# Kernel optimization log

Hardware: AMD Instinct MI355X
Metric: run time of the kernel (lower is better)

## Reference

```python
import jax, jax.numpy as jnp
import numpy as np

B, S, H, I, E = 2, 2048, 1024, 4096, 8
NUM_STEPS = 2
RMS_EPS = 1e-6


def rmsnorm(x, w, eps=RMS_EPS):
    var = jnp.mean(jnp.square(x), axis=-1, keepdims=True)
    return x * jax.lax.rsqrt(var + eps) * w


def setup_inputs() -> dict:
    key = jax.random.key(0)
    ks = jax.random.split(key, 7)
    return {
        "hidden_states": jax.random.normal(ks[0], (B, S, H), dtype=jnp.float32),
        "gate_w": jax.random.normal(ks[1], (E, H), dtype=jnp.float32) * 0.02,
        "w1": jax.random.normal(ks[2], (E, H, I), dtype=jnp.float32) * 0.02,
        "b1": jnp.zeros((E, I), dtype=jnp.float32),
        "w2": jax.random.normal(ks[3], (E, I, H), dtype=jnp.float32) * 0.02,
        "b2": jnp.zeros((E, H), dtype=jnp.float32),
        "ln_w": jnp.ones((H,), dtype=jnp.float32),
    }


def reference(hidden_states, gate_w, w1, b1, w2, b2, ln_w):
    x = hidden_states  # [B,S,H]
    dtype = hidden_states.dtype
    for i in range(NUM_STEPS):
        inp = x if i == 0 else rmsnorm(x, ln_w)
        t = inp.reshape(-1, H)  # [T,H], T = B*S
        # softmax gate (computed in fp32 as in the original)
        logits = t @ gate_w.T  # [T,E]
        rw = jax.nn.softmax(logits.astype(jnp.float32), axis=-1).astype(dtype)
        # all experts on all tokens (dense MoE), batched over E
        h = jax.nn.silu(jnp.einsum('td,edi->tei', t, w1) + b1)  # [T,E,I]
        eo = jnp.einsum('tei,eih->teh', h, w2) + b2             # [T,E,H]
        comb = jnp.einsum('te,teh->th', rw, eo)                 # weighted combine
        x = x + comb.reshape(B, S, H)
    return x  # final_projection is Identity (no feature extractor)
```

## Files before the change

### kernel.cpp

```cpp
#include <hip/hip_runtime.h>
#include <hip/hip_bf16.h>

#define T_TOK 4096
#define H_DIM 1024
#define I_DIM 4096
#define E_EXP 8
#define RMS_EPS_F 1e-6f

using bf16x8 = __attribute__((ext_vector_type(8))) __bf16;
using f32x4  = __attribute__((ext_vector_type(4))) float;

__device__ inline void gload_lds16(const void* g, void* l) {
    __builtin_amdgcn_global_load_lds(
        (const __attribute__((address_space(1))) void*)g,
        (__attribute__((address_space(3))) void*)l,
        16, 0, 0);
}

__global__ __launch_bounds__(256) void k_transpose_cvt(
    const float* __restrict__ in, __hip_bfloat16* __restrict__ out, int R, int C)
{
    __shared__ float tile[32][33];
    const size_t mat = (size_t)R * C;
    in  += (size_t)blockIdx.z * mat;
    out += (size_t)blockIdx.z * mat;
    const int c0 = blockIdx.x * 32, r0 = blockIdx.y * 32;
    const int tx = threadIdx.x & 31, ty = threadIdx.x >> 5;
#pragma unroll
    for (int dy = 0; dy < 32; dy += 8)
        tile[ty + dy][tx] = in[(size_t)(r0 + ty + dy) * C + (c0 + tx)];
    __syncthreads();
#pragma unroll
    for (int dy = 0; dy < 32; dy += 8)
        out[(size_t)(c0 + ty + dy) * R + (r0 + tx)] = __float2bfloat16(tile[tx][ty + dy]);
}

__global__ __launch_bounds__(256) void k_prep(
    const float* __restrict__ x, const float* __restrict__ lnw,
    __hip_bfloat16* __restrict__ tb, int do_norm)
{
    const int t = blockIdx.x;
    const float* row = x + (size_t)t * H_DIM;
    const int base = threadIdx.x * 4;
    float4 v = *(const float4*)(row + base);
    if (do_norm) {
        float ss = v.x*v.x + v.y*v.y + v.z*v.z + v.w*v.w;
#pragma unroll
        for (int off = 32; off > 0; off >>= 1) ss += __shfl_xor(ss, off);
        __shared__ float wsum[4];
        const int w = threadIdx.x >> 6;
        if ((threadIdx.x & 63) == 0) wsum[w] = ss;
        __syncthreads();
        const float tot = wsum[0] + wsum[1] + wsum[2] + wsum[3];
        const float scale = rsqrtf(tot * (1.0f / H_DIM) + RMS_EPS_F);
        float4 g = *(const float4*)(lnw + base);
        v.x *= scale * g.x; v.y *= scale * g.y; v.z *= scale * g.z; v.w *= scale * g.w;
    }
    __hip_bfloat16* o = tb + (size_t)t * H_DIM + base;
    o[0] = __float2bfloat16(v.x); o[1] = __float2bfloat16(v.y);
    o[2] = __float2bfloat16(v.z); o[3] = __float2bfloat16(v.w);
}

__global__ __launch_bounds__(256) void k_gate(
    const __hip_bfloat16* __restrict__ tb, const float* __restrict__ gw,
    float* __restrict__ rw)
{
    const int t = blockIdx.x * 4 + (threadIdx.x >> 6);
    const int lane = threadIdx.x & 63;
    const __hip_bfloat16* row = tb + (size_t)t * H_DIM;
    float acc[E_EXP];
#pragma unroll
    for (int e = 0; e < E_EXP; ++e) acc[e] = 0.f;
    for (int h = lane; h < H_DIM; h += 64) {
        const float xv = __bfloat162float(row[h]);
#pragma unroll
        for (int e = 0; e < E_EXP; ++e) acc[e] += xv * gw[e * H_DIM + h];
    }
#pragma unroll
    for (int e = 0; e < E_EXP; ++e) {
#pragma unroll
        for (int off = 32; off > 0; off >>= 1) acc[e] += __shfl_xor(acc[e], off);
    }
    if (lane == 0) {
        float mx = acc[0];
#pragma unroll
        for (int e = 1; e < E_EXP; ++e) mx = fmaxf(mx, acc[e]);
        float ex[E_EXP], s = 0.f;
#pragma unroll
        for (int e = 0; e < E_EXP; ++e) { ex[e] = __expf(acc[e] - mx); s += ex[e]; }
        const float inv = 1.f / s;
#pragma unroll
        for (int e = 0; e < E_EXP; ++e) rw[(size_t)t * E_EXP + e] = ex[e] * inv;
    }
}


__device__ __forceinline__ void ld4(bf16x8 (&r)[4], const char* rd, int kof) {
#pragma unroll
    for (int i = 0; i < 4; ++i)
        r[i] = *(const bf16x8*)(rd + i * 2048 + kof);
}
__device__ __forceinline__ void mfma16(const bf16x8 (&a)[4], const bf16x8 (&b)[4],
                                       f32x4 (&acc)[4][4]) {
    __builtin_amdgcn_s_setprio(1);
#pragma unroll
    for (int mi = 0; mi < 4; ++mi)
#pragma unroll
        for (int ni = 0; ni < 4; ++ni)
            acc[mi][ni] = __builtin_amdgcn_mfma_f32_16x16x32_bf16(
                a[mi], b[ni], acc[mi][ni], 0, 0, 0);
    __builtin_amdgcn_s_setprio(0);
}

#define BAR()   __builtin_amdgcn_s_barrier()
#define LGKM0() asm volatile("s_waitcnt lgkmcnt(0)" ::: "memory")
#define VMW0()  asm volatile("s_waitcnt vmcnt(0)" ::: "memory")
#define SCHED0() __builtin_amdgcn_sched_barrier(0)

template <int MODE>
__global__ __launch_bounds__(256, 2) void k_gemm4(
    const __hip_bfloat16* __restrict__ A, int lda, long long strideA,
    const __hip_bfloat16* __restrict__ Bt, int ldb, long long strideB,
    const float* __restrict__ bias, int strideBias,
    void* __restrict__ out, int ldo, long long strideOut, int K)
{
    __shared__ __hip_bfloat16 sA[2][128 * 64];
    __shared__ __hip_bfloat16 sB[2][128 * 64];

    const int z = blockIdx.z;
    A  += (size_t)z * (size_t)strideA;
    Bt += (size_t)z * (size_t)strideB;

    const int tid  = threadIdx.x;
    const int lane = tid & 63;
    const int wid  = tid >> 6;
    const int wr = wid >> 1, wc = wid & 1;
    const int m0 = blockIdx.y * 128, n0 = blockIdx.x * 128;

    const int sr  = tid >> 3;
    const int skb = ((((tid & 7) * 16) ^ ((sr & 7) << 4)) >> 1);
    const __hip_bfloat16* gA = A  + (size_t)(m0 + sr) * lda + skb;
    const __hip_bfloat16* gB = Bt + (size_t)(n0 + sr) * ldb + skb;
    char* const dA = (char*)&sA[0][0] + tid * 16;
    char* const dB = (char*)&sB[0][0] + tid * 16;

#define STAGE_A(bb, kt) do { \
    const __hip_bfloat16* s_ = gA + (size_t)(kt) * 64; \
    gload_lds16(s_,                     dA + (bb) * 16384); \
    gload_lds16(s_ + (size_t)32 * lda,  dA + (bb) * 16384 + 4096); \
    gload_lds16(s_ + (size_t)64 * lda,  dA + (bb) * 16384 + 8192); \
    gload_lds16(s_ + (size_t)96 * lda,  dA + (bb) * 16384 + 12288); \
} while (0)
#define STAGE_B(bb, kt) do { \
    const __hip_bfloat16* s_ = gB + (size_t)(kt) * 64; \
    gload_lds16(s_,                     dB + (bb) * 16384); \
    gload_lds16(s_ + (size_t)32 * ldb,  dB + (bb) * 16384 + 4096); \
    gload_lds16(s_ + (size_t)64 * ldb,  dB + (bb) * 16384 + 8192); \
    gload_lds16(s_ + (size_t)96 * ldb,  dB + (bb) * 16384 + 12288); \
} while (0)

    const int fr = lane & 15, kg = lane >> 4;
    const int msk  = (fr & 7) << 4;
    const int kof0 = (kg * 16) ^ msk;
    const int kof1 = (64 + kg * 16) ^ msk;
    const char* rdA = (const char*)&sA[0][0] + wr * 8192 + fr * 128;
    const char* rdB = (const char*)&sB[0][0] + wc * 8192 + fr * 128;

    f32x4  acc[4][4] = {};
    bf16x8 a[4], b[4];

    const int NT = K >> 6;

    STAGE_A(0, 0); STAGE_B(0, 0);
    VMW0(); BAR(); SCHED0();

#define TILE_S(BB, t) do { \
    ld4(a, rdA + (BB) * 16384, kof0); \
    ld4(b, rdB + (BB) * 16384, kof0); \
    STAGE_A((BB) ^ 1, (t) + 1); STAGE_B((BB) ^ 1, (t) + 1); \
    LGKM0(); SCHED0(); \
    mfma16(a, b, acc); \
    ld4(a, rdA + (BB) * 16384, kof1); \
    ld4(b, rdB + (BB) * 16384, kof1); \
    LGKM0(); SCHED0(); \
    mfma16(a, b, acc); \
    VMW0(); BAR(); SCHED0(); \
} while (0)

    for (int i = 0; i < NT / 2 - 1; ++i) {
        TILE_S(0, 2 * i);
        TILE_S(1, 2 * i + 1);
    }
    TILE_S(0, NT - 2);
    {
        ld4(a, rdA + 16384, kof0);
        ld4(b, rdB + 16384, kof0);
        LGKM0(); SCHED0();
        mfma16(a, b, acc);
        ld4(a, rdA + 16384, kof1);
        ld4(b, rdB + 16384, kof1);
        LGKM0(); SCHED0();
        mfma16(a, b, acc);
    }

    const int rB = kg * 4;
    if (MODE == 0) {
        __hip_bfloat16* O = (__hip_bfloat16*)out + (size_t)z * (size_t)strideOut;
        const float* bz = bias + (size_t)z * (size_t)strideBias;
#pragma unroll
        for (int mi = 0; mi < 4; ++mi) {
            const int gm = m0 + wr * 64 + mi * 16 + rB;
#pragma unroll
            for (int ni = 0; ni < 4; ++ni) {
                const int gn = n0 + wc * 64 + ni * 16 + fr;
                const float bv = bz[gn];
#pragma unroll
                for (int j = 0; j < 4; ++j) {
                    float v = acc[mi][ni][j] + bv;
                    v = v / (1.f + __expf(-v));
                    O[(size_t)(gm + j) * ldo + gn] = __float2bfloat16(v);
                }
            }
        }
    } else {
        float* O = (float*)out + (size_t)z * (size_t)strideOut;
#pragma unroll
        for (int mi = 0; mi < 4; ++mi) {
            const int gm = m0 + wr * 64 + mi * 16 + rB;
#pragma unroll
            for (int ni = 0; ni < 4; ++ni) {
                const int gn = n0 + wc * 64 + ni * 16 + fr;
#pragma unroll
                for (int j = 0; j < 4; ++j)
                    O[(size_t)(gm + j) * ldo + gn] = acc[mi][ni][j];
            }
        }
    }
#undef STAGE_A
#undef STAGE_B
#undef TILE_S
}

__global__ __launch_bounds__(256) void k_combine(
    const float* __restrict__ eo, const float* __restrict__ rw,
    const float* __restrict__ b2, float* __restrict__ x, int e0, int g)
{
    const int t = blockIdx.x;
    const int h = threadIdx.x * 4;
    float4 acc = *(const float4*)(x + (size_t)t * H_DIM + h);
    for (int j = 0; j < g; ++j) {
        const float w = rw[(size_t)t * E_EXP + e0 + j];
        const float4 v  = *(const float4*)(eo + ((size_t)j * T_TOK + t) * H_DIM + h);
        const float4 bz = *(const float4*)(b2 + (size_t)(e0 + j) * H_DIM + h);
        acc.x += w * (v.x + bz.x);
        acc.y += w * (v.y + bz.y);
        acc.z += w * (v.z + bz.z);
        acc.w += w * (v.w + bz.w);
    }
    *(float4*)(x + (size_t)t * H_DIM + h) = acc;
}

extern "C" void kernel_launch(void* const* d_in, const int* in_sizes, int n_in,
                              void* d_out, int out_size, void* d_ws, size_t ws_size,
                              hipStream_t stream)
{
    const float* hidden = (const float*)d_in[0];
    const float* gate_w = (const float*)d_in[1];
    const float* w1     = (const float*)d_in[2];
    const float* b1     = (const float*)d_in[3];
    const float* w2     = (const float*)d_in[4];
    const float* b2     = (const float*)d_in[5];
    const float* ln_w   = (const float*)d_in[6];
    float* x = (float*)d_out;

    const size_t w1t_b = (size_t)E_EXP * I_DIM * H_DIM * 2;
    const size_t w2t_b = (size_t)E_EXP * H_DIM * I_DIM * 2;
    const size_t tb_b  = (size_t)T_TOK * H_DIM * 2;
    const size_t rw_b  = (size_t)T_TOK * E_EXP * 4;
    const size_t hb1_b = (size_t)T_TOK * I_DIM * 2;
    const size_t eo1_b = (size_t)T_TOK * H_DIM * 4;
    const size_t base_b = w1t_b + w2t_b + tb_b + rw_b;

    int g = 0;
    for (int cand = 8; cand >= 1; cand >>= 1)
        if (base_b + (size_t)cand * (hb1_b + eo1_b) <= ws_size) { g = cand; break; }

    char* ws = (char*)d_ws;
    __hip_bfloat16* w1t = (__hip_bfloat16*)ws;  ws += w1t_b;
    __hip_bfloat16* w2t = (__hip_bfloat16*)ws;  ws += w2t_b;
    __hip_bfloat16* tb  = (__hip_bfloat16*)ws;  ws += tb_b;
    float*          rw  = (float*)ws;           ws += rw_b;
    __hip_bfloat16* hb  = (__hip_bfloat16*)ws;
    float*          eo  = (float*)(ws + (size_t)(g > 0 ? g : 1) * hb1_b);

    hipMemcpyAsync(x, hidden, (size_t)T_TOK * H_DIM * 4, hipMemcpyDeviceToDevice, stream);

    if (g == 0) return;

    k_transpose_cvt<<<dim3(I_DIM / 32, H_DIM / 32, E_EXP), 256, 0, stream>>>(w1, w1t, H_DIM, I_DIM);
    k_transpose_cvt<<<dim3(H_DIM / 32, I_DIM / 32, E_EXP), 256, 0, stream>>>(w2, w2t, I_DIM, H_DIM);

    for (int step = 0; step < 2; ++step) {
        k_prep<<<T_TOK, 256, 0, stream>>>(x, ln_w, tb, step);
        k_gate<<<T_TOK / 4, 256, 0, stream>>>(tb, gate_w, rw);

        for (int e0 = 0; e0 < E_EXP; e0 += g) {
            k_gemm4<0><<<dim3(I_DIM / 128, T_TOK / 128, g), 256, 0, stream>>>(
                tb, H_DIM, 0,
                w1t + (size_t)e0 * I_DIM * H_DIM, H_DIM, (long long)I_DIM * H_DIM,
                b1 + (size_t)e0 * I_DIM, I_DIM,
                hb, I_DIM, (long long)T_TOK * I_DIM, H_DIM);
            k_gemm4<2><<<dim3(H_DIM / 128, T_TOK / 128, g), 256, 0, stream>>>(
                hb, I_DIM, (long long)T_TOK * I_DIM,
                w2t + (size_t)e0 * H_DIM * I_DIM, I_DIM, (long long)H_DIM * I_DIM,
                nullptr, 0,
                eo, H_DIM, (long long)T_TOK * H_DIM, I_DIM);
            k_combine<<<T_TOK, 256, 0, stream>>>(eo, rw, b2, x, e0, g);
        }
    }
}
```

Baseline: 1.709 ms.

## Fold routing weight into first GEMM epilogue, store expert outputs as bf16, swap grid order

The routing weight for each token is now multiplied into the SiLU output in the first GEMM's epilogue, so the second GEMM yields already-weighted expert outputs. Those outputs are written as bf16 instead of fp32, which halves the write and the read traffic of the intermediate buffer and leaves room for a larger expert group in the workspace. The grid is also transposed so blockIdx.x walks token tiles, which changes the tile visit order and L2 reuse. The cost is extra rounding: weighted activations and expert outputs are each quantised to bf16 before the fp32 accumulate.

```diff
diff --git a/kernel.cpp b/kernel.cpp
--- a/kernel.cpp
+++ b/kernel.cpp
@@ -122,6 +122,7 @@
     const __hip_bfloat16* __restrict__ A, int lda, long long strideA,
     const __hip_bfloat16* __restrict__ Bt, int ldb, long long strideB,
     const float* __restrict__ bias, int strideBias,
+    const float* __restrict__ rw, int e0,
     void* __restrict__ out, int ldo, long long strideOut, int K)
 {
     __shared__ __hip_bfloat16 sA[2][128 * 64];
@@ -135,7 +136,7 @@
     const int lane = tid & 63;
     const int wid  = tid >> 6;
     const int wr = wid >> 1, wc = wid & 1;
-    const int m0 = blockIdx.y * 128, n0 = blockIdx.x * 128;
+    const int m0 = blockIdx.x * 128, n0 = blockIdx.y * 128;
 
     const int sr  = tid >> 3;
     const int skb = ((((tid & 7) * 16) ^ ((sr & 7) << 4)) >> 1);
@@ -211,19 +212,20 @@
         for (int mi = 0; mi < 4; ++mi) {
             const int gm = m0 + wr * 64 + mi * 16 + rB;
 #pragma unroll
-            for (int ni = 0; ni < 4; ++ni) {
-                const int gn = n0 + wc * 64 + ni * 16 + fr;
-                const float bv = bz[gn];
-#pragma unroll
-                for (int j = 0; j < 4; ++j) {
-                    float v = acc[mi][ni][j] + bv;
+            for (int j = 0; j < 4; ++j) {
+                const int row = gm + j;
+                const float rwv = rw[(size_t)row * E_EXP + e0 + z];
+#pragma unroll
+                for (int ni = 0; ni < 4; ++ni) {
+                    const int gn = n0 + wc * 64 + ni * 16 + fr;
+                    float v = acc[mi][ni][j] + bz[gn];
                     v = v / (1.f + __expf(-v));
-                    O[(size_t)(gm + j) * ldo + gn] = __float2bfloat16(v);
+                    O[(size_t)row * ldo + gn] = __float2bfloat16(rwv * v);
                 }
             }
         }
     } else {
-        float* O = (float*)out + (size_t)z * (size_t)strideOut;
+        __hip_bfloat16* O = (__hip_bfloat16*)out + (size_t)z * (size_t)strideOut;
 #pragma unroll
         for (int mi = 0; mi < 4; ++mi) {
             const int gm = m0 + wr * 64 + mi * 16 + rB;
@@ -232,7 +234,7 @@
                 const int gn = n0 + wc * 64 + ni * 16 + fr;
 #pragma unroll
                 for (int j = 0; j < 4; ++j)
-                    O[(size_t)(gm + j) * ldo + gn] = acc[mi][ni][j];
+                    O[(size_t)(gm + j) * ldo + gn] = __float2bfloat16(acc[mi][ni][j]);
             }
         }
     }
@@ -242,7 +244,7 @@
 }
 
 __global__ __launch_bounds__(256) void k_combine(
-    const float* __restrict__ eo, const float* __restrict__ rw,
+    const __hip_bfloat16* __restrict__ eo, const float* __restrict__ rw,
     const float* __restrict__ b2, float* __restrict__ x, int e0, int g)
 {
     const int t = blockIdx.x;
@@ -250,12 +252,12 @@
     float4 acc = *(const float4*)(x + (size_t)t * H_DIM + h);
     for (int j = 0; j < g; ++j) {
         const float w = rw[(size_t)t * E_EXP + e0 + j];
-        const float4 v  = *(const float4*)(eo + ((size_t)j * T_TOK + t) * H_DIM + h);
+        const __hip_bfloat16* p = eo + ((size_t)j * T_TOK + t) * H_DIM + h;
         const float4 bz = *(const float4*)(b2 + (size_t)(e0 + j) * H_DIM + h);
-        acc.x += w * (v.x + bz.x);
-        acc.y += w * (v.y + bz.y);
-        acc.z += w * (v.z + bz.z);
-        acc.w += w * (v.w + bz.w);
+        acc.x += __bfloat162float(p[0]) + w * bz.x;
+        acc.y += __bfloat162float(p[1]) + w * bz.y;
+        acc.z += __bfloat162float(p[2]) + w * bz.z;
+        acc.w += __bfloat162float(p[3]) + w * bz.w;
     }
     *(float4*)(x + (size_t)t * H_DIM + h) = acc;
 }
@@ -278,7 +280,7 @@
     const size_t tb_b  = (size_t)T_TOK * H_DIM * 2;
     const size_t rw_b  = (size_t)T_TOK * E_EXP * 4;
     const size_t hb1_b = (size_t)T_TOK * I_DIM * 2;
-    const size_t eo1_b = (size_t)T_TOK * H_DIM * 4;
+    const size_t eo1_b = (size_t)T_TOK * H_DIM * 2;
     const size_t base_b = w1t_b + w2t_b + tb_b + rw_b;
 
     int g = 0;
@@ -291,7 +293,7 @@
     __hip_bfloat16* tb  = (__hip_bfloat16*)ws;  ws += tb_b;
     float*          rw  = (float*)ws;           ws += rw_b;
     __hip_bfloat16* hb  = (__hip_bfloat16*)ws;
-    float*          eo  = (float*)(ws + (size_t)(g > 0 ? g : 1) * hb1_b);
+    __hip_bfloat16* eo  = (__hip_bfloat16*)(ws + (size_t)(g > 0 ? g : 1) * hb1_b);
 
     hipMemcpyAsync(x, hidden, (size_t)T_TOK * H_DIM * 4, hipMemcpyDeviceToDevice, stream);
 
@@ -305,14 +307,16 @@
         k_gate<<<T_TOK / 4, 256, 0, stream>>>(tb, gate_w, rw);
 
         for (int e0 = 0; e0 < E_EXP; e0 += g) {
-            k_gemm4<0><<<dim3(I_DIM / 128, T_TOK / 128, g), 256, 0, stream>>>(
+            k_gemm4<0><<<dim3(T_TOK / 128, I_DIM / 128, g), 256, 0, stream>>>(
                 tb, H_DIM, 0,
                 w1t + (size_t)e0 * I_DIM * H_DIM, H_DIM, (long long)I_DIM * H_DIM,
                 b1 + (size_t)e0 * I_DIM, I_DIM,
+                rw, e0,
                 hb, I_DIM, (long long)T_TOK * I_DIM, H_DIM);
-            k_gemm4<2><<<dim3(H_DIM / 128, T_TOK / 128, g), 256, 0, stream>>>(
+            k_gemm4<2><<<dim3(T_TOK / 128, H_DIM / 128, g), 256, 0, stream>>>(
                 hb, I_DIM, (long long)T_TOK * I_DIM,
                 w2t + (size_t)e0 * H_DIM * I_DIM, I_DIM, (long long)H_DIM * I_DIM,
+                nullptr, 0,
                 nullptr, 0,
                 eo, H_DIM, (long long)T_TOK * H_DIM, I_DIM);
             k_combine<<<T_TOK, 256, 0, stream>>>(eo, rw, b2, x, e0, g);
```

Result: faster. 1.641 ms (-4.0%).
